# Kernel optimization log

Hardware: AMD Instinct MI355X
Metric: run time of the kernel (lower is better)

Reference implementation:

```python
import jax, jax.numpy as jnp
import numpy as np

N_GROUPS = 2048   # n: number of ragged groups (graph instances)
L = 64            # l: padded context length per group
NQ = 8192         # nq.sum(): total queries
DQ = 512          # d_q = 2*d_h (concat src/dst)
DK = 256          # d_k = d_h
DV = 256          # d   = d_h (value dim)
DZ = 256          # d_z = d_h (attention dim)


def setup_inputs() -> dict:
    key = jax.random.key(0)
    ks = jax.random.split(key, 8)
    q = jax.random.normal(ks[0], (NQ, DQ), dtype=jnp.float32)
    k = jax.random.normal(ks[1], (N_GROUPS, L, DK), dtype=jnp.float32)
    v = jax.random.normal(ks[2], (N_GROUPS, L, DV), dtype=jnp.float32)
    # boolean validity mask; ensure at least one valid slot per group so softmax is finite
    m = jax.random.bernoulli(ks[3], 0.5, (N_GROUPS, L)).at[:, 0].set(True)
    # per-query group index: jit-friendly equivalent of repeat_interleave(nq, 0)
    gidx = jnp.sort(jax.random.randint(ks[4], (NQ,), 0, N_GROUPS))
    Wq = jax.random.normal(ks[5], (DQ, DZ), dtype=jnp.float32) / np.float32(np.sqrt(DQ))
    bq = jnp.zeros((DZ,), dtype=jnp.float32)
    Wk = jax.random.normal(ks[6], (DK, DZ), dtype=jnp.float32) / np.float32(np.sqrt(DK))
    bk = jnp.zeros((DZ,), dtype=jnp.float32)
    return dict(q=q, k=k, v=v, m=m, gidx=gidx, Wq=Wq, bq=bq, Wk=Wk, bk=bk)


def reference(q, k, v, m, gidx, Wq, bq, Wk, bk):
    # q: (NQ, DQ); k: (n, L, DK); v: (n, L, DV); m: (n, L) bool; gidx: (NQ,) int
    qz = q @ Wq + bq                                   # (NQ, DZ)
    kz = jnp.einsum('nlk,kz->nlz', k, Wk) + bk         # (n, L, DZ)
    # gather per-query context (== repeat_interleave(nq, 0) in the torch code)
    kg = kz[gidx]                                      # (NQ, L, DZ)
    vg = v[gidx]                                       # (NQ, L, DV)
    mg = m[gidx]                                       # (NQ, L)
    scale = np.float32(1.0 / np.sqrt(DZ))
    s = jnp.einsum('qlz,qz->ql', kg, qz) * scale       # (NQ, L)
    s = jnp.where(mg, s, -jnp.inf)                     # masked_fill(~m, -inf)
    p = jax.nn.softmax(s, axis=1)                      # softmax over context length
    return jnp.einsum('qld,ql->qd', vg, p)             # (NQ, DV)
```

## Files before the change

### kernel.cpp

```cpp
#include <hip/hip_runtime.h>
#include <hip/hip_bf16.h>

#define NQ 8192
#define NG 2048
#define CTX 64
#define DQ 512
#define DK 256
#define DV 256
#define DZ 256

typedef __attribute__((ext_vector_type(8))) short short8;
typedef __attribute__((ext_vector_type(4))) float f32x4;

__device__ __forceinline__ unsigned short f2bf_bits(float f) {
  __hip_bfloat16 h = __float2bfloat16(f);
  return __builtin_bit_cast(unsigned short, h);
}
__device__ __forceinline__ float bf2f(unsigned short u) {
  unsigned int x = ((unsigned int)u) << 16;
  return __builtin_bit_cast(float, x);
}
__device__ __forceinline__ void split2(float x, unsigned short& h, unsigned short& l) {
  h = f2bf_bits(x);
  l = f2bf_bits(x - bf2f(h));
}
__device__ __forceinline__ void cvt8_hl(f32x4 f0, f32x4 f1, short8& h8, short8& l8) {
#pragma unroll
  for (int j = 0; j < 4; j++) { unsigned short h, l; split2(f0[j], h, l); h8[j] = (short)h; l8[j] = (short)l; }
#pragma unroll
  for (int j = 0; j < 4; j++) { unsigned short h, l; split2(f1[j], h, l); h8[4 + j] = (short)h; l8[4 + j] = (short)l; }
}
__device__ __forceinline__ short8 cvt8_h(f32x4 f0, f32x4 f1) {
  short8 h8;
#pragma unroll
  for (int j = 0; j < 4; j++) h8[j] = (short)f2bf_bits(f0[j]);
#pragma unroll
  for (int j = 0; j < 4; j++) h8[4 + j] = (short)f2bf_bits(f1[j]);
  return h8;
}

__global__ void prep_kernel(const float* __restrict__ Wq, const float* __restrict__ Wk,
                            const int* __restrict__ gidx,
                            unsigned short* __restrict__ WqTh, unsigned short* __restrict__ WqTl,
                            unsigned short* __restrict__ Wkh, unsigned short* __restrict__ Wkl,
                            int* __restrict__ starts, int* __restrict__ mflag)
{
  int t = blockIdx.x * 256 + threadIdx.x;
  if (t < DZ * DQ) {
    int z = t >> 9, kq = t & 511;
    unsigned short h, l; split2(Wq[(size_t)kq * DZ + z], h, l);
    WqTh[t] = h; WqTl[t] = l;
  } else if (t < DZ * DQ + DK * DZ) {
    int u = t - DZ * DQ;
    unsigned short h, l; split2(Wk[u], h, l);
    Wkh[u] = h; Wkl[u] = l;
  } else if (t < DZ * DQ + DK * DZ + NG + 1) {
    int g = t - (DZ * DQ + DK * DZ);
    int lo = 0, hi = NQ;
    while (lo < hi) { int mid = (lo + hi) >> 1; if (gidx[mid] < g) lo = mid + 1; else hi = mid; }
    starts[g] = lo;
  } else if (t == DZ * DQ + DK * DZ + NG + 1) {
    mflag[0] = 0;
  }
}

__global__ void maskscan_kernel(const unsigned int* __restrict__ mw, int* __restrict__ flag)
{
  int i = blockIdx.x * 256 + threadIdx.x;
  unsigned int w = mw[i];
  bool bad = (w != 0u && w != 1u && w != 0x3F800000u);
  if (__any(bad) && ((threadIdx.x & 63) == 0))
    atomicOr(flag, 1);
}

__global__ __launch_bounds__(256, 4) void qz_kernel(
    const float* __restrict__ q, const float* __restrict__ bq,
    const unsigned short* __restrict__ WqTh, const unsigned short* __restrict__ WqTl,
    unsigned short* __restrict__ qzh, unsigned short* __restrict__ qzl)
{
  const int tid = threadIdx.x;
  const int wave = tid >> 6, lane = tid & 63;
  const int i16 = lane & 15, hi4 = lane >> 4;
  const int mbase = blockIdx.x * 32;

  f32x4 acc[2][4];
#pragma unroll
  for (int a = 0; a < 2; a++)
#pragma unroll
    for (int b = 0; b < 4; b++) acc[a][b] = {0.f, 0.f, 0.f, 0.f};

  for (int kk = 0; kk < DQ; kk += 32) {
    f32x4 araw[2][2];
#pragma unroll
    for (int mt = 0; mt < 2; mt++) {
      const float* src = q + (size_t)(mbase + mt * 16 + i16) * DQ + kk + hi4 * 8;
      araw[mt][0] = *reinterpret_cast<const f32x4*>(src);
      araw[mt][1] = *reinterpret_cast<const f32x4*>(src + 4);
    }
    short8 ah[2], al[2];
#pragma unroll
    for (int mt = 0; mt < 2; mt++) cvt8_hl(araw[mt][0], araw[mt][1], ah[mt], al[mt]);

#pragma unroll
    for (int ntp = 0; ntp < 2; ntp++) {
      short8 bh[2], bl[2];
#pragma unroll
      for (int j = 0; j < 2; j++) {
        const int n = wave * 64 + (ntp * 2 + j) * 16 + i16;
        bh[j] = *reinterpret_cast<const short8*>(WqTh + (size_t)n * DQ + kk + hi4 * 8);
        bl[j] = *reinterpret_cast<const short8*>(WqTl + (size_t)n * DQ + kk + hi4 * 8);
      }
#pragma unroll
      for (int mt = 0; mt < 2; mt++)
#pragma unroll
        for (int j = 0; j < 2; j++) {
          f32x4 a = acc[mt][ntp * 2 + j];
          a = __builtin_amdgcn_mfma_f32_16x16x32_bf16(ah[mt], bh[j], a, 0, 0, 0);
          a = __builtin_amdgcn_mfma_f32_16x16x32_bf16(al[mt], bh[j], a, 0, 0, 0);
          a = __builtin_amdgcn_mfma_f32_16x16x32_bf16(ah[mt], bl[j], a, 0, 0, 0);
          acc[mt][ntp * 2 + j] = a;
        }
    }
  }

  const float scale = 0.0625f;
#pragma unroll
  for (int nt = 0; nt < 4; nt++) {
    const int n = wave * 64 + nt * 16 + i16;
    const float bias = bq[n];
#pragma unroll
    for (int mt = 0; mt < 2; mt++)
#pragma unroll
      for (int r = 0; r < 4; r++) {
        const int m = mbase + mt * 16 + hi4 * 4 + r;
        float x = (acc[mt][nt][r] + bias) * scale;
        unsigned short h, l; split2(x, h, l);
        qzh[(size_t)m * DZ + n] = h;
        qzl[(size_t)m * DZ + n] = l;
      }
  }
}

__global__ __launch_bounds__(256, 4) void qk_kernel(
    const unsigned short* __restrict__ qzh, const unsigned short* __restrict__ qzl,
    const unsigned short* __restrict__ Wkh, const unsigned short* __restrict__ Wkl,
    unsigned short* __restrict__ qkh, unsigned short* __restrict__ qkl)
{
  const int tid = threadIdx.x;
  const int wave = tid >> 6, lane = tid & 63;
  const int i16 = lane & 15, hi4 = lane >> 4;
  const int mbase = blockIdx.x * 32;

  f32x4 acc[2][4];
#pragma unroll
  for (int a = 0; a < 2; a++)
#pragma unroll
    for (int b = 0; b < 4; b++) acc[a][b] = {0.f, 0.f, 0.f, 0.f};

#pragma unroll
  for (int kk = 0; kk < DZ; kk += 32) {
    short8 ah[2], al[2];
#pragma unroll
    for (int mt = 0; mt < 2; mt++) {
      ah[mt] = *reinterpret_cast<const short8*>(qzh + (size_t)(mbase + mt * 16 + i16) * DZ + kk + hi4 * 8);
      al[mt] = *reinterpret_cast<const short8*>(qzl + (size_t)(mbase + mt * 16 + i16) * DZ + kk + hi4 * 8);
    }
#pragma unroll
    for (int ntp = 0; ntp < 2; ntp++) {
      short8 bh[2], bl[2];
#pragma unroll
      for (int j = 0; j < 2; j++) {
        const int n = wave * 64 + (ntp * 2 + j) * 16 + i16;
        bh[j] = *reinterpret_cast<const short8*>(Wkh + (size_t)n * DZ + kk + hi4 * 8);
        bl[j] = *reinterpret_cast<const short8*>(Wkl + (size_t)n * DZ + kk + hi4 * 8);
      }
#pragma unroll
      for (int mt = 0; mt < 2; mt++)
#pragma unroll
        for (int j = 0; j < 2; j++) {
          f32x4 a = acc[mt][ntp * 2 + j];
          a = __builtin_amdgcn_mfma_f32_16x16x32_bf16(ah[mt], bh[j], a, 0, 0, 0);
          a = __builtin_amdgcn_mfma_f32_16x16x32_bf16(al[mt], bh[j], a, 0, 0, 0);
          a = __builtin_amdgcn_mfma_f32_16x16x32_bf16(ah[mt], bl[j], a, 0, 0, 0);
          acc[mt][ntp * 2 + j] = a;
        }
    }
  }

#pragma unroll
  for (int nt = 0; nt < 4; nt++) {
    const int n = wave * 64 + nt * 16 + i16;
#pragma unroll
    for (int mt = 0; mt < 2; mt++)
#pragma unroll
      for (int r = 0; r < 4; r++) {
        const int mrow = mbase + mt * 16 + hi4 * 4 + r;
        unsigned short h, l; split2(acc[mt][nt][r], h, l);
        qkh[(size_t)mrow * DK + n] = h;
        qkl[(size_t)mrow * DK + n] = l;
      }
  }
}

__global__ __launch_bounds__(256, 3) void attn_qk_kernel(
    const float* __restrict__ kmat, const float* __restrict__ vmat,
    const void* __restrict__ mmask, const int* __restrict__ mflagp,
    const int* __restrict__ starts,
    const unsigned short* __restrict__ qkh, const unsigned short* __restrict__ qkl,
    float* __restrict__ out)
{
  const int g = blockIdx.x;
  const int q0 = starts[g];
  const int q1 = starts[g + 1];
  if (q0 >= q1) return;

  const int tid = threadIdx.x;
  const int wave = tid >> 6, lane = tid & 63;
  const int i16 = lane & 15, hi4 = lane >> 4;

  __shared__ __align__(16) unsigned short k_lds[CTX * DK];
  __shared__ __align__(16) unsigned short ph_lds[CTX * 16];
  __shared__ __align__(16) unsigned short pl_lds[CTX * 16];
  __shared__ float maskbias[CTX];

  if (tid < CTX) {
    bool valid;
    if (mflagp[0])
      valid = ((const unsigned char*)mmask)[(size_t)g * CTX + tid] != 0;
    else
      valid = ((const unsigned int*)mmask)[(size_t)g * CTX + tid] != 0u;
    maskbias[tid] = valid ? 0.0f : -1e30f;
  }

  const float* kg = kmat + (size_t)g * (CTX * DK);
#pragma unroll
  for (int it = 0; it < 8; it++) {
    const int flat = it * 2048 + tid * 8;
    const int row = flat >> 8, col = flat & 255;
    f32x4 f0 = *reinterpret_cast<const f32x4*>(kg + flat);
    f32x4 f1 = *reinterpret_cast<const f32x4*>(kg + flat + 4);
    short8 h8 = cvt8_h(f0, f1);
    const int boff = (row * 512 + col * 2) ^ ((row & 7) << 4);
    *reinterpret_cast<short8*>(reinterpret_cast<char*>(k_lds) + boff) = h8;
  }

  const float* vg = vmat + (size_t)g * (CTX * DV);
  short8 vb[2][4];
#pragma unroll
  for (int kt = 0; kt < 2; kt++)
#pragma unroll
    for (int nt = 0; nt < 4; nt++) {
      const int d = wave * 64 + nt * 16 + i16;
      const float* vcol = vg + (size_t)(kt * 32 + hi4 * 8) * DV + d;
      short8 t;
#pragma unroll
      for (int j = 0; j < 8; j++) t[j] = (short)f2bf_bits(vcol[(size_t)j * DV]);
      vb[kt][nt] = t;
    }

  __syncthreads();
  float mb[16];
#pragma unroll
  for (int mt = 0; mt < 4; mt++)
#pragma unroll
    for (int r = 0; r < 4; r++)
      mb[mt * 4 + r] = maskbias[mt * 16 + hi4 * 4 + r];

  const int nchunks = (q1 - q0 + 15) >> 4;

  for (int c = 0; c < nchunks; c++) {
    const int qbase = q0 + c * 16;
    f32x4 accs[4];
#pragma unroll
    for (int mt = 0; mt < 4; mt++) accs[mt] = {0.f, 0.f, 0.f, 0.f};

    int qrow = qbase + i16; if (qrow > NQ - 1) qrow = NQ - 1;
    const unsigned short* qh_p = qkh + (size_t)qrow * DK;
    const unsigned short* ql_p = qkl + (size_t)qrow * DK;
#pragma unroll
    for (int kk = 0; kk < DK; kk += 32) {
      short8 bfh = *reinterpret_cast<const short8*>(qh_p + kk + hi4 * 8);
      short8 bfl = *reinterpret_cast<const short8*>(ql_p + kk + hi4 * 8);
#pragma unroll
      for (int mt = 0; mt < 4; mt++) {
        const int mrow = mt * 16 + i16;
        const int boff = (mrow * 512 + (kk + hi4 * 8) * 2) ^ ((mrow & 7) << 4);
        short8 af = *reinterpret_cast<const short8*>(reinterpret_cast<const char*>(k_lds) + boff);
        accs[mt] = __builtin_amdgcn_mfma_f32_16x16x32_bf16(af, bfh, accs[mt], 0, 0, 0);
        accs[mt] = __builtin_amdgcn_mfma_f32_16x16x32_bf16(af, bfl, accs[mt], 0, 0, 0);
      }
    }

    float mx = -3.0e38f;
#pragma unroll
    for (int mt = 0; mt < 4; mt++)
#pragma unroll
      for (int r = 0; r < 4; r++) {
        float s = accs[mt][r] + mb[mt * 4 + r];
        accs[mt][r] = s;
        mx = fmaxf(mx, s);
      }
    mx = fmaxf(mx, __shfl_xor(mx, 16));
    mx = fmaxf(mx, __shfl_xor(mx, 32));
    float sum = 0.f;
#pragma unroll
    for (int mt = 0; mt < 4; mt++)
#pragma unroll
      for (int r = 0; r < 4; r++) {
        float p = __expf(accs[mt][r] - mx);
        accs[mt][r] = p;
        sum += p;
      }
    sum += __shfl_xor(sum, 16);
    sum += __shfl_xor(sum, 32);
    const float inv = 1.0f / sum;

    __syncthreads();
#pragma unroll
    for (int mt = 0; mt < 4; mt++)
#pragma unroll
      for (int r = 0; r < 4; r++) {
        const int mrow = mt * 16 + hi4 * 4 + r;
        unsigned short h, l; split2(accs[mt][r] * inv, h, l);
        ph_lds[mrow * 16 + i16] = h;
        pl_lds[mrow * 16 + i16] = l;
      }

    f32x4 acco[4];
#pragma unroll
    for (int nt = 0; nt < 4; nt++) acco[nt] = {0.f, 0.f, 0.f, 0.f};
#pragma unroll
    for (int kt = 0; kt < 2; kt++) {
      short8 pah, pal;
#pragma unroll
      for (int j = 0; j < 8; j++) {
        pah[j] = (short)ph_lds[(kt * 32 + hi4 * 8 + j) * 16 + i16];
        pal[j] = (short)pl_lds[(kt * 32 + hi4 * 8 + j) * 16 + i16];
      }
#pragma unroll
      for (int nt = 0; nt < 4; nt++) {
        acco[nt] = __builtin_amdgcn_mfma_f32_16x16x32_bf16(pah, vb[kt][nt], acco[nt], 0, 0, 0);
        acco[nt] = __builtin_amdgcn_mfma_f32_16x16x32_bf16(pal, vb[kt][nt], acco[nt], 0, 0, 0);
      }
    }

#pragma unroll
    for (int nt = 0; nt < 4; nt++) {
      const int d = wave * 64 + nt * 16 + i16;
#pragma unroll
      for (int r = 0; r < 4; r++) {
        const int qrow2 = qbase + hi4 * 4 + r;
        if (qrow2 < q1)
          out[(size_t)qrow2 * DV + d] = acco[nt][r];
      }
    }
  }
}

extern "C" void kernel_launch(void* const* d_in, const int* in_sizes, int n_in,
                              void* d_out, int out_size, void* d_ws, size_t ws_size,
                              hipStream_t stream) {
  const float* q  = (const float*)d_in[0];
  const float* k  = (const float*)d_in[1];
  const float* v  = (const float*)d_in[2];
  const void*  m  = d_in[3];
  const int* gidx = (const int*)d_in[4];
  const float* Wq = (const float*)d_in[5];
  const float* bq = (const float*)d_in[6];
  const float* Wk = (const float*)d_in[7];
  float* out = (float*)d_out;

  char* ws = (char*)d_ws;
  unsigned short* qzh  = (unsigned short*)(ws);
  unsigned short* qzl  = (unsigned short*)(ws + 4194304);
  unsigned short* qkh  = (unsigned short*)(ws + 8388608);
  unsigned short* qkl  = (unsigned short*)(ws + 12582912);
  unsigned short* WqTh = (unsigned short*)(ws + 16777216);
  unsigned short* WqTl = (unsigned short*)(ws + 17039360);
  unsigned short* Wkh  = (unsigned short*)(ws + 17301504);
  unsigned short* Wkl  = (unsigned short*)(ws + 17432576);
  int* starts          = (int*)(ws + 17563648);
  int* mflag           = (int*)(ws + 17571844);

  hipLaunchKernelGGL(prep_kernel, dim3(777), dim3(256), 0, stream,
                     Wq, Wk, gidx, WqTh, WqTl, Wkh, Wkl, starts, mflag);
  hipLaunchKernelGGL(maskscan_kernel, dim3(128), dim3(256), 0, stream,
                     (const unsigned int*)m, mflag);
  hipLaunchKernelGGL(qz_kernel, dim3(NQ / 32), dim3(256), 0, stream,
                     q, bq, WqTh, WqTl, qzh, qzl);
  hipLaunchKernelGGL(qk_kernel, dim3(NQ / 32), dim3(256), 0, stream,
                     qzh, qzl, Wkh, Wkl, qkh, qkl);
  hipLaunchKernelGGL(attn_qk_kernel, dim3(NG), dim3(256), 0, stream,
                     k, v, m, (const int*)mflag, starts, qkh, qkl, out);
}
```

Baseline: 115.6 us.

## Assign one group per wave in attention kernel, drop LDS staging

The attention kernel now maps one group to each wave (four groups per block) instead of one group per 256-thread block. K and V are read straight from global memory into MFMA fragments rather than being staged in LDS. The softmax probabilities are redistributed across lanes with ds_bpermute instead of an LDS round trip behind __syncthreads. This removes block-level barriers and LDS traffic and raises the number of independent groups in flight. In exchange, groups with several query chunks re-read K and V from global/cache on every chunk, and the strided V column loads may coalesce poorly.

```diff
diff --git a/kernel.cpp b/kernel.cpp
--- a/kernel.cpp
+++ b/kernel.cpp
@@ -11,6 +11,7 @@
 
 typedef __attribute__((ext_vector_type(8))) short short8;
 typedef __attribute__((ext_vector_type(4))) float f32x4;
+typedef __attribute__((ext_vector_type(4))) unsigned int u32x4;
 
 __device__ __forceinline__ unsigned short f2bf_bits(float f) {
   __hip_bfloat16 h = __float2bfloat16(f);
@@ -202,92 +203,66 @@
   }
 }
 
-__global__ __launch_bounds__(256, 3) void attn_qk_kernel(
+__global__ __launch_bounds__(256, 3) void attn_pw_kernel(
     const float* __restrict__ kmat, const float* __restrict__ vmat,
     const void* __restrict__ mmask, const int* __restrict__ mflagp,
     const int* __restrict__ starts,
     const unsigned short* __restrict__ qkh, const unsigned short* __restrict__ qkl,
     float* __restrict__ out)
 {
-  const int g = blockIdx.x;
-  const int q0 = starts[g];
-  const int q1 = starts[g + 1];
+  const int wave = threadIdx.x >> 6, lane = threadIdx.x & 63;
+  const int q16 = lane & 15, h = lane >> 4;
+  const int g = blockIdx.x * 4 + wave;
+  const int q0 = starts[g], q1 = starts[g + 1];
   if (q0 >= q1) return;
 
-  const int tid = threadIdx.x;
-  const int wave = tid >> 6, lane = tid & 63;
-  const int i16 = lane & 15, hi4 = lane >> 4;
-
-  __shared__ __align__(16) unsigned short k_lds[CTX * DK];
-  __shared__ __align__(16) unsigned short ph_lds[CTX * 16];
-  __shared__ __align__(16) unsigned short pl_lds[CTX * 16];
-  __shared__ float maskbias[CTX];
-
-  if (tid < CTX) {
-    bool valid;
-    if (mflagp[0])
-      valid = ((const unsigned char*)mmask)[(size_t)g * CTX + tid] != 0;
-    else
-      valid = ((const unsigned int*)mmask)[(size_t)g * CTX + tid] != 0u;
-    maskbias[tid] = valid ? 0.0f : -1e30f;
-  }
+  unsigned int mbits = 0;
+  const int mfl = mflagp[0];
+#pragma unroll
+  for (int mt = 0; mt < 4; mt++)
+#pragma unroll
+    for (int r = 0; r < 4; r++) {
+      const int l = mt * 16 + 4 * h + r;
+      bool valid;
+      if (mfl) valid = ((const unsigned char*)mmask)[(size_t)g * CTX + l] != 0;
+      else     valid = ((const unsigned int*)mmask)[(size_t)g * CTX + l] != 0u;
+      mbits |= (valid ? 1u : 0u) << (mt * 4 + r);
+    }
 
   const float* kg = kmat + (size_t)g * (CTX * DK);
-#pragma unroll
-  for (int it = 0; it < 8; it++) {
-    const int flat = it * 2048 + tid * 8;
-    const int row = flat >> 8, col = flat & 255;
-    f32x4 f0 = *reinterpret_cast<const f32x4*>(kg + flat);
-    f32x4 f1 = *reinterpret_cast<const f32x4*>(kg + flat + 4);
-    short8 h8 = cvt8_h(f0, f1);
-    const int boff = (row * 512 + col * 2) ^ ((row & 7) << 4);
-    *reinterpret_cast<short8*>(reinterpret_cast<char*>(k_lds) + boff) = h8;
-  }
-
   const float* vg = vmat + (size_t)g * (CTX * DV);
-  short8 vb[2][4];
-#pragma unroll
-  for (int kt = 0; kt < 2; kt++)
-#pragma unroll
-    for (int nt = 0; nt < 4; nt++) {
-      const int d = wave * 64 + nt * 16 + i16;
-      const float* vcol = vg + (size_t)(kt * 32 + hi4 * 8) * DV + d;
-      short8 t;
-#pragma unroll
-      for (int j = 0; j < 8; j++) t[j] = (short)f2bf_bits(vcol[(size_t)j * DV]);
-      vb[kt][nt] = t;
-    }
-
-  __syncthreads();
-  float mb[16];
-#pragma unroll
-  for (int mt = 0; mt < 4; mt++)
-#pragma unroll
-    for (int r = 0; r < 4; r++)
-      mb[mt * 4 + r] = maskbias[mt * 16 + hi4 * 4 + r];
-
   const int nchunks = (q1 - q0 + 15) >> 4;
 
   for (int c = 0; c < nchunks; c++) {
     const int qbase = q0 + c * 16;
+    int qrow = qbase + q16; if (qrow > NQ - 1) qrow = NQ - 1;
+    const unsigned short* qh_p = qkh + (size_t)qrow * DK + h * 8;
+    const unsigned short* ql_p = qkl + (size_t)qrow * DK + h * 8;
+
+    short8 bfh[8], bfl[8];
+#pragma unroll
+    for (int kk = 0; kk < 8; kk++) {
+      bfh[kk] = *reinterpret_cast<const short8*>(qh_p + kk * 32);
+      bfl[kk] = *reinterpret_cast<const short8*>(ql_p + kk * 32);
+    }
+
     f32x4 accs[4];
 #pragma unroll
     for (int mt = 0; mt < 4; mt++) accs[mt] = {0.f, 0.f, 0.f, 0.f};
-
-    int qrow = qbase + i16; if (qrow > NQ - 1) qrow = NQ - 1;
-    const unsigned short* qh_p = qkh + (size_t)qrow * DK;
-    const unsigned short* ql_p = qkl + (size_t)qrow * DK;
-#pragma unroll
-    for (int kk = 0; kk < DK; kk += 32) {
-      short8 bfh = *reinterpret_cast<const short8*>(qh_p + kk + hi4 * 8);
-      short8 bfl = *reinterpret_cast<const short8*>(ql_p + kk + hi4 * 8);
+#pragma unroll
+    for (int kk = 0; kk < 8; kk++) {
+      short8 kf[4];
 #pragma unroll
       for (int mt = 0; mt < 4; mt++) {
-        const int mrow = mt * 16 + i16;
-        const int boff = (mrow * 512 + (kk + hi4 * 8) * 2) ^ ((mrow & 7) << 4);
-        short8 af = *reinterpret_cast<const short8*>(reinterpret_cast<const char*>(k_lds) + boff);
-        accs[mt] = __builtin_amdgcn_mfma_f32_16x16x32_bf16(af, bfh, accs[mt], 0, 0, 0);
-        accs[mt] = __builtin_amdgcn_mfma_f32_16x16x32_bf16(af, bfl, accs[mt], 0, 0, 0);
+        const float* rowp = kg + (size_t)(mt * 16 + q16) * DK + kk * 32 + h * 8;
+        f32x4 f0 = *reinterpret_cast<const f32x4*>(rowp);
+        f32x4 f1 = *reinterpret_cast<const f32x4*>(rowp + 4);
+        kf[mt] = cvt8_h(f0, f1);
+      }
+#pragma unroll
+      for (int mt = 0; mt < 4; mt++) {
+        accs[mt] = __builtin_amdgcn_mfma_f32_16x16x32_bf16(kf[mt], bfh[kk], accs[mt], 0, 0, 0);
+        accs[mt] = __builtin_amdgcn_mfma_f32_16x16x32_bf16(kf[mt], bfl[kk], accs[mt], 0, 0, 0);
       }
     }
 
@@ -296,7 +271,7 @@
     for (int mt = 0; mt < 4; mt++)
 #pragma unroll
       for (int r = 0; r < 4; r++) {
-        float s = accs[mt][r] + mb[mt * 4 + r];
+        float s = accs[mt][r] + (((mbits >> (mt * 4 + r)) & 1u) ? 0.0f : -1e30f);
         accs[mt][r] = s;
         mx = fmaxf(mx, s);
       }
@@ -315,43 +290,86 @@
     sum += __shfl_xor(sum, 32);
     const float inv = 1.0f / sum;
 
-    __syncthreads();
-#pragma unroll
-    for (int mt = 0; mt < 4; mt++)
+    unsigned int w0h[4], w1h[4], w0l[4], w1l[4];
+#pragma unroll
+    for (int mt = 0; mt < 4; mt++) {
+      unsigned short hh[4], ll[4];
 #pragma unroll
       for (int r = 0; r < 4; r++) {
-        const int mrow = mt * 16 + hi4 * 4 + r;
-        unsigned short h, l; split2(accs[mt][r] * inv, h, l);
-        ph_lds[mrow * 16 + i16] = h;
-        pl_lds[mrow * 16 + i16] = l;
-      }
-
-    f32x4 acco[4];
-#pragma unroll
-    for (int nt = 0; nt < 4; nt++) acco[nt] = {0.f, 0.f, 0.f, 0.f};
+        float pn = accs[mt][r] * inv;
+        split2(pn, hh[r], ll[r]);
+      }
+      w0h[mt] = (unsigned int)hh[0] | ((unsigned int)hh[1] << 16);
+      w1h[mt] = (unsigned int)hh[2] | ((unsigned int)hh[3] << 16);
+      w0l[mt] = (unsigned int)ll[0] | ((unsigned int)ll[1] << 16);
+      w1l[mt] = (unsigned int)ll[2] | ((unsigned int)ll[3] << 16);
+    }
+
+    const int hb = h >> 1;
+    const int sl0 = (q16 + 16 * ((2 * h) & 3)) << 2;
+    const int sl1 = (q16 + 16 * ((2 * h + 1) & 3)) << 2;
+    short8 pah[2], pal[2];
 #pragma unroll
     for (int kt = 0; kt < 2; kt++) {
-      short8 pah, pal;
-#pragma unroll
-      for (int j = 0; j < 8; j++) {
-        pah[j] = (short)ph_lds[(kt * 32 + hi4 * 8 + j) * 16 + i16];
-        pal[j] = (short)pl_lds[(kt * 32 + hi4 * 8 + j) * 16 + i16];
+      u32x4 bh_, bl_;
+      unsigned int e, o;
+      e = (unsigned int)__builtin_amdgcn_ds_bpermute(sl0, (int)w0h[2 * kt]);
+      o = (unsigned int)__builtin_amdgcn_ds_bpermute(sl0, (int)w0h[2 * kt + 1]);
+      bh_[0] = hb ? o : e;
+      e = (unsigned int)__builtin_amdgcn_ds_bpermute(sl0, (int)w1h[2 * kt]);
+      o = (unsigned int)__builtin_amdgcn_ds_bpermute(sl0, (int)w1h[2 * kt + 1]);
+      bh_[1] = hb ? o : e;
+      e = (unsigned int)__builtin_amdgcn_ds_bpermute(sl1, (int)w0h[2 * kt]);
+      o = (unsigned int)__builtin_amdgcn_ds_bpermute(sl1, (int)w0h[2 * kt + 1]);
+      bh_[2] = hb ? o : e;
+      e = (unsigned int)__builtin_amdgcn_ds_bpermute(sl1, (int)w1h[2 * kt]);
+      o = (unsigned int)__builtin_amdgcn_ds_bpermute(sl1, (int)w1h[2 * kt + 1]);
+      bh_[3] = hb ? o : e;
+
+      e = (unsigned int)__builtin_amdgcn_ds_bpermute(sl0, (int)w0l[2 * kt]);
+      o = (unsigned int)__builtin_amdgcn_ds_bpermute(sl0, (int)w0l[2 * kt + 1]);
+      bl_[0] = hb ? o : e;
+      e = (unsigned int)__builtin_amdgcn_ds_bpermute(sl0, (int)w1l[2 * kt]);
+      o = (unsigned int)__builtin_amdgcn_ds_bpermute(sl0, (int)w1l[2 * kt + 1]);
+      bl_[1] = hb ? o : e;
+      e = (unsigned int)__builtin_amdgcn_ds_bpermute(sl1, (int)w0l[2 * kt]);
+      o = (unsigned int)__builtin_amdgcn_ds_bpermute(sl1, (int)w0l[2 * kt + 1]);
+      bl_[2] = hb ? o : e;
+      e = (unsigned int)__builtin_amdgcn_ds_bpermute(sl1, (int)w1l[2 * kt]);
+      o = (unsigned int)__builtin_amdgcn_ds_bpermute(sl1, (int)w1l[2 * kt + 1]);
+      bl_[3] = hb ? o : e;
+
+      pah[kt] = __builtin_bit_cast(short8, bh_);
+      pal[kt] = __builtin_bit_cast(short8, bl_);
+    }
+
+#pragma unroll
+    for (int dp = 0; dp < 4; dp++) {
+      f32x4 acco[4];
+#pragma unroll
+      for (int nt = 0; nt < 4; nt++) acco[nt] = {0.f, 0.f, 0.f, 0.f};
+#pragma unroll
+      for (int kt = 0; kt < 2; kt++) {
+        const float* vrow = vg + (size_t)(kt * 32 + h * 8) * DV + dp * 64 + q16;
+#pragma unroll
+        for (int nt = 0; nt < 4; nt++) {
+          const float* vcol = vrow + nt * 16;
+          short8 vb;
+#pragma unroll
+          for (int j = 0; j < 8; j++) vb[j] = (short)f2bf_bits(vcol[(size_t)j * DV]);
+          acco[nt] = __builtin_amdgcn_mfma_f32_16x16x32_bf16(pah[kt], vb, acco[nt], 0, 0, 0);
+          acco[nt] = __builtin_amdgcn_mfma_f32_16x16x32_bf16(pal[kt], vb, acco[nt], 0, 0, 0);
+        }
       }
 #pragma unroll
       for (int nt = 0; nt < 4; nt++) {
-        acco[nt] = __builtin_amdgcn_mfma_f32_16x16x32_bf16(pah, vb[kt][nt], acco[nt], 0, 0, 0);
-        acco[nt] = __builtin_amdgcn_mfma_f32_16x16x32_bf16(pal, vb[kt][nt], acco[nt], 0, 0, 0);
-      }
-    }
-
-#pragma unroll
-    for (int nt = 0; nt < 4; nt++) {
-      const int d = wave * 64 + nt * 16 + i16;
-#pragma unroll
-      for (int r = 0; r < 4; r++) {
-        const int qrow2 = qbase + hi4 * 4 + r;
-        if (qrow2 < q1)
-          out[(size_t)qrow2 * DV + d] = acco[nt][r];
+        const int d = dp * 64 + nt * 16 + q16;
+#pragma unroll
+        for (int r = 0; r < 4; r++) {
+          const int qrow2 = qbase + h * 4 + r;
+          if (qrow2 < q1)
+            out[(size_t)qrow2 * DV + d] = acco[nt][r];
+        }
       }
     }
   }
@@ -390,6 +408,6 @@
                      q, bq, WqTh, WqTl, qzh, qzl);
   hipLaunchKernelGGL(qk_kernel, dim3(NQ / 32), dim3(256), 0, stream,
                      qzh, qzl, Wkh, Wkl, qkh, qkl);
-  hipLaunchKernelGGL(attn_qk_kernel, dim3(NG), dim3(256), 0, stream,
+  hipLaunchKernelGGL(attn_pw_kernel, dim3(NG / 4), dim3(256), 0, stream,
                      k, v, m, (const int*)mflag, starts, qkh, qkl, out);
 }
```

New measurement: 172.9 us. 1.5x slower.
